# Performance work log

Hardware: AMD Instinct MI355X
Metric: run time of the kernel (lower is better)

Reference implementation:

```python
import jax, jax.numpy as jnp
import numpy as np

LOOKBACK = 1
LOOKAHEAD = 0
SEQ, BATCH, IN, HID = 1024, 16, 1024, 1024
K = LOOKBACK + 1 + LOOKAHEAD


def quick_gelu(x):
    return x * jax.nn.sigmoid(1.702 * x)


def setup_inputs() -> dict:
    key = jax.random.key(0)
    ks = jax.random.split(key, 5)
    scale = 1.0 / np.sqrt(IN * K)  # like torch Conv1d default init scale
    X = jax.random.normal(ks[0], (SEQ, BATCH, IN), dtype=jnp.float32)
    Wz = jax.random.normal(ks[1], (HID, IN, K), dtype=jnp.float32) * scale
    bz = jax.random.normal(ks[2], (HID,), dtype=jnp.float32) * scale
    Wf = jax.random.normal(ks[3], (HID, IN, K), dtype=jnp.float32) * scale
    bf = jax.random.normal(ks[4], (HID,), dtype=jnp.float32) * scale
    return {"X": X, "Wz": Wz, "bz": bz, "Wf": Wf, "bf": bf}


def _conv1d(x_pad, W, b):
    # x_pad: (B, Cin, T+K-1), W: (Cout, Cin, K) -> (B, Cout, T)
    y = jax.lax.conv_general_dilated(
        x_pad, W, window_strides=(1,), padding="VALID",
        dimension_numbers=("NCH", "OIH", "NCH"))
    return y + b[None, :, None]


def reference(X, Wz, bz, Wf, bf):
    # pad time dim: lookback zeros before, lookahead zeros after
    X_pad = jnp.pad(X, ((LOOKBACK, LOOKAHEAD), (0, 0), (0, 0)))
    X_pad = jnp.transpose(X_pad, (1, 2, 0))  # (B, Cin, T+K-1)
    Z = jnp.transpose(_conv1d(X_pad, Wz, bz), (2, 0, 1))  # (T, B, H)
    F = jnp.transpose(_conv1d(X_pad, Wf, bf), (2, 0, 1))  # (T, B, H)
    Z = quick_gelu(Z)
    F = jax.nn.sigmoid(F)

    def step(h, fz):
        f, z = fz
        h = f * z + (1.0 - f) * h
        return h, h

    h0 = jnp.zeros((BATCH, HID), dtype=X.dtype)
    _, H = jax.lax.scan(step, h0, (F, Z))  # H: (T, B, HID)
    return H, H[-1:, :, :]
```

## Files before the change

kernel.cpp:

```cpp
#include <hip/hip_runtime.h>
#include <stdint.h>

#define T_SEQ 1024
#define B_SZ  16
#define C_IN  1024
#define C_HID 1024
#define M_ROWS (T_SEQ * B_SZ)
#define N_COLS (2 * C_HID)
#define K_DIM  (2 * C_IN)

#define NCHUNK 16
#define CLEN   (T_SEQ / NCHUNK)
#define NBH    (B_SZ * C_HID)

typedef __attribute__((ext_vector_type(8))) short bf16x8;
typedef __attribute__((ext_vector_type(4))) float f32x4;
typedef unsigned short u16;

#define MFMA __builtin_amdgcn_mfma_f32_16x16x32_bf16

__device__ __forceinline__ u16 f2bf(float f) {
  union { float f; unsigned u; } v; v.f = f;
  unsigned r = v.u + 0x7fffu + ((v.u >> 16) & 1u);
  return (u16)(r >> 16);
}
__device__ __forceinline__ float bf2f(unsigned s) {
  union { unsigned u; float f; } v; v.u = s << 16;
  return v.f;
}

__device__ __forceinline__ void async_cp16(const u16* g, u16* l) {
  __builtin_amdgcn_global_load_lds(
      (const __attribute__((address_space(1))) unsigned*)(uintptr_t)g,
      (__attribute__((address_space(3))) unsigned*)(uintptr_t)l,
      16, 0, 0);
}

__global__ void k_convert_x(const float* __restrict__ X, u16* __restrict__ Xp) {
  int i = blockIdx.x * 256 + threadIdx.x;
  const int total4 = (M_ROWS + B_SZ) * C_IN / 4;
  if (i >= total4) return;
  int e = i << 2;
  const int PAD = B_SZ * C_IN;
  ushort4 o;
  if (e < PAD) {
    o.x = o.y = o.z = o.w = 0;
  } else {
    float4 v = *reinterpret_cast<const float4*>(X + (e - PAD));
    o.x = f2bf(v.x); o.y = f2bf(v.y); o.z = f2bf(v.z); o.w = f2bf(v.w);
  }
  *reinterpret_cast<ushort4*>(Xp + e) = o;
}

__global__ void k_repack_w(const float* __restrict__ Wz, const float* __restrict__ Wf,
                           u16* __restrict__ Wt) {
  int i = blockIdx.x * 256 + threadIdx.x;
  if (i >= 2 * 1024 * 1024) return;
  int g  = i >> 20;
  int hc = i & ((1 << 20) - 1);
  int h  = hc >> 10;
  int c  = hc & 1023;
  const float* W = g ? Wf : Wz;
  float2 w = *reinterpret_cast<const float2*>(W + ((size_t)(h << 10) + c) * 2);
  size_t n = ((size_t)h << 1) | (size_t)g;
  Wt[n * K_DIM + c]        = f2bf(w.x);
  Wt[n * K_DIM + 1024 + c] = f2bf(w.y);
}

__global__ __launch_bounds__(512, 2) void k_gemm8(const u16* __restrict__ Xp,
                                                  const u16* __restrict__ Wt,
                                                  const float* __restrict__ bz,
                                                  const float* __restrict__ bfv,
                                                  u16* __restrict__ Cb) {
  __shared__ u16 lds[2][2][2][8192];
  const int tid  = threadIdx.x;
  const int lane = tid & 63;
  const int wid  = tid >> 6;
  const int wr = wid >> 2;
  const int wc = wid & 3;
  const int lr = lane & 15;

  int wg = (blockIdx.x & 7) * 64 + (blockIdx.x >> 3);
  const int m0 = (wg >> 3) << 8;
  const int n0 = (wg & 7) << 8;

  const int p    = tid << 4;
  const int q    = p ^ (((p >> 7) & 7) << 4);
  const int grow = q >> 7;
  const int gcol = (q & 127) >> 1;
  const int ldsw = (tid >> 6) << 9;

  const int rbase = lr << 6;
  int co[2];
#pragma unroll
  for (int ks = 0; ks < 2; ++ks)
    co[ks] = ((((ks << 6) | ((lane >> 4) << 4)) ^ ((lr & 7) << 4)) >> 1);

  auto stage = [&](int j) {
    int kt = j >> 2, part = j & 3, buf = kt & 1;
    if (part >= 2) {
      int h = part - 2;
      const u16* g = Xp + (size_t)(m0 + (h << 7) + grow + ((kt >= 16) ? B_SZ : 0)) * C_IN
                        + ((kt & 15) << 6) + gcol;
      u16* l = &lds[buf][0][h][ldsw];
      async_cp16(g, l);
      async_cp16(g + (size_t)64 * C_IN, l + 4096);
    } else {
      const u16* g = Wt + (size_t)(n0 + (part << 7) + grow) * K_DIM + (kt << 6) + gcol;
      u16* l = &lds[buf][1][part][ldsw];
      async_cp16(g, l);
      async_cp16(g + (size_t)64 * K_DIM, l + 4096);
    }
  };

  f32x4 acc[8][4] = {};
  bf16x8 a[4][2], b0[2][2], b1[2][2];

  for (int j = 0; j < 7; ++j) stage(j);
  asm volatile("s_waitcnt vmcnt(6)" ::: "memory");
  __builtin_amdgcn_s_barrier();

#pragma unroll 2
  for (int t = 0; t < 32; ++t) {
    const int buf = t & 1;
    const u16* pA = &lds[buf][0][wr][0];
    const u16* pB = &lds[buf][1][wc >> 1][(wc & 1) << 12];
    const int jb = 4 * t + 7;

#pragma unroll
    for (int mi = 0; mi < 4; ++mi)
#pragma unroll
      for (int ks = 0; ks < 2; ++ks)
        a[mi][ks] = *(const bf16x8*)(pA + (mi << 10) + rbase + co[ks]);
#pragma unroll
    for (int ni = 0; ni < 2; ++ni)
#pragma unroll
      for (int ks = 0; ks < 2; ++ks)
        b0[ni][ks] = *(const bf16x8*)(pB + (ni << 10) + rbase + co[ks]);
    if (jb < 128) stage(jb);
    __builtin_amdgcn_s_barrier();
    asm volatile("s_waitcnt lgkmcnt(0)" ::: "memory");
    __builtin_amdgcn_s_setprio(1);
#pragma unroll
    for (int mi = 0; mi < 4; ++mi)
#pragma unroll
      for (int ni = 0; ni < 2; ++ni)
#pragma unroll
        for (int ks = 0; ks < 2; ++ks)
          acc[mi][ni] = MFMA(a[mi][ks], b0[ni][ks], acc[mi][ni], 0, 0, 0);
    __builtin_amdgcn_s_setprio(0);
    __builtin_amdgcn_s_barrier();

#pragma unroll
    for (int ni = 0; ni < 2; ++ni)
#pragma unroll
      for (int ks = 0; ks < 2; ++ks)
        b1[ni][ks] = *(const bf16x8*)(pB + ((2 + ni) << 10) + rbase + co[ks]);
    if (jb + 1 < 128) stage(jb + 1);
    __builtin_amdgcn_s_barrier();
    asm volatile("s_waitcnt lgkmcnt(0)" ::: "memory");
    __builtin_amdgcn_s_setprio(1);
#pragma unroll
    for (int mi = 0; mi < 4; ++mi)
#pragma unroll
      for (int ni = 0; ni < 2; ++ni)
#pragma unroll
        for (int ks = 0; ks < 2; ++ks)
          acc[mi][2 + ni] = MFMA(a[mi][ks], b1[ni][ks], acc[mi][2 + ni], 0, 0, 0);
    __builtin_amdgcn_s_setprio(0);
    __builtin_amdgcn_s_barrier();

#pragma unroll
    for (int mi = 0; mi < 4; ++mi)
#pragma unroll
      for (int ks = 0; ks < 2; ++ks)
        a[mi][ks] = *(const bf16x8*)(pA + ((4 + mi) << 10) + rbase + co[ks]);
    if (jb + 2 < 128) stage(jb + 2);
    __builtin_amdgcn_s_barrier();
    asm volatile("s_waitcnt lgkmcnt(0)" ::: "memory");
    __builtin_amdgcn_s_setprio(1);
#pragma unroll
    for (int mi = 0; mi < 4; ++mi)
#pragma unroll
      for (int ni = 0; ni < 2; ++ni)
#pragma unroll
        for (int ks = 0; ks < 2; ++ks)
          acc[4 + mi][2 + ni] = MFMA(a[mi][ks], b1[ni][ks], acc[4 + mi][2 + ni], 0, 0, 0);
    __builtin_amdgcn_s_setprio(0);
    __builtin_amdgcn_s_barrier();

    if (jb + 3 < 128) stage(jb + 3);
    if (t < 30) asm volatile("s_waitcnt vmcnt(6)" ::: "memory");
    else        asm volatile("s_waitcnt vmcnt(0)" ::: "memory");
    __builtin_amdgcn_s_barrier();
    __builtin_amdgcn_s_setprio(1);
#pragma unroll
    for (int mi = 0; mi < 4; ++mi)
#pragma unroll
      for (int ni = 0; ni < 2; ++ni)
#pragma unroll
        for (int ks = 0; ks < 2; ++ks)
          acc[4 + mi][ni] = MFMA(a[mi][ks], b0[ni][ks], acc[4 + mi][ni], 0, 0, 0);
    __builtin_amdgcn_s_setprio(0);
    __builtin_amdgcn_s_barrier();
  }

  const int colp = lane & 15;
  const bool isz = (colp & 1) == 0;
  const float kk = isz ? 1.702f : 1.0f;
  const int hbase = (n0 + (wc << 6) + colp) >> 1;
  const int fmb = (m0 >> 4) + (wr << 3);
  const int fnb = (n0 >> 4) + (wc << 2);
#pragma unroll
  for (int ni = 0; ni < 4; ++ni) {
    float bias = isz ? bz[hbase + 8 * ni] : bfv[hbase + 8 * ni];
#pragma unroll
    for (int mi = 0; mi < 8; ++mi) {
      ushort4 o;
#pragma unroll
      for (int r = 0; r < 4; ++r) {
        float v = acc[mi][ni][r] + bias;
        float s = 1.f / (1.f + __expf(-kk * v));
        ((u16*)&o)[r] = f2bf(isz ? v * s : s);
      }
      size_t fi = (size_t)(fmb + mi) * 128 + (fnb + ni);
      *reinterpret_cast<ushort4*>(Cb + fi * 256 + (lane << 2)) = o;
    }
  }
}

__global__ __launch_bounds__(256) void k_scan1(const u16* __restrict__ Cb,
                                               float* __restrict__ Ap,
                                               float* __restrict__ Bp) {
  int i = blockIdx.x * 256 + threadIdx.x;
  int h  = i & (C_HID - 1);
  int b4 = (i >> 10) & 3;
  int c  = i >> 12;
  const size_t lane_off = (size_t)(h >> 3) * 256 + b4 * 64 + (h & 7) * 8;
  float hh[4] = {0.f, 0.f, 0.f, 0.f}, P[4] = {1.f, 1.f, 1.f, 1.f};
#pragma unroll 8
  for (int tt = 0; tt < CLEN; ++tt) {
    size_t t = (size_t)c * CLEN + tt;
    uint4 v = *reinterpret_cast<const uint4*>(Cb + t * 32768 + lane_off);
    float z[4] = {bf2f(v.x & 0xffffu), bf2f(v.x >> 16),
                  bf2f(v.y & 0xffffu), bf2f(v.y >> 16)};
    float f[4] = {bf2f(v.z & 0xffffu), bf2f(v.z >> 16),
                  bf2f(v.w & 0xffffu), bf2f(v.w >> 16)};
#pragma unroll
    for (int r = 0; r < 4; ++r) {
      hh[r] += f[r] * (z[r] - hh[r]);
      P[r]  *= (1.f - f[r]);
    }
  }
  *reinterpret_cast<f32x4*>(Ap + (size_t)i * 4) = (f32x4){hh[0], hh[1], hh[2], hh[3]};
  *reinterpret_cast<f32x4*>(Bp + (size_t)i * 4) = (f32x4){P[0], P[1], P[2], P[3]};
}

__global__ __launch_bounds__(256) void k_scan2(const float* __restrict__ Ap,
                                               const float* __restrict__ Bp,
                                               float* __restrict__ St) {
  int j = blockIdx.x * 256 + threadIdx.x;
  float hh[4] = {0.f, 0.f, 0.f, 0.f};
#pragma unroll
  for (int c = 0; c < NCHUNK; ++c) {
    size_t idx = ((size_t)c * 4096 + j) * 4;
    *reinterpret_cast<f32x4*>(St + idx) = (f32x4){hh[0], hh[1], hh[2], hh[3]};
    f32x4 A = *reinterpret_cast<const f32x4*>(Ap + idx);
    f32x4 B = *reinterpret_cast<const f32x4*>(Bp + idx);
#pragma unroll
    for (int r = 0; r < 4; ++r) hh[r] = A[r] + B[r] * hh[r];
  }
}

__global__ __launch_bounds__(256) void k_scan3(const u16* __restrict__ Cb,
                                               const float* __restrict__ St,
                                               float* __restrict__ out) {
  int i = blockIdx.x * 256 + threadIdx.x;
  int h  = i & (C_HID - 1);
  int b4 = (i >> 10) & 3;
  int c  = i >> 12;
  const size_t lane_off = (size_t)(h >> 3) * 256 + b4 * 64 + (h & 7) * 8;
  f32x4 s = *reinterpret_cast<const f32x4*>(St + (size_t)i * 4);
  float hh[4] = {s[0], s[1], s[2], s[3]};
#pragma unroll 8
  for (int tt = 0; tt < CLEN; ++tt) {
    size_t t = (size_t)c * CLEN + tt;
    uint4 v = *reinterpret_cast<const uint4*>(Cb + t * 32768 + lane_off);
    float z[4] = {bf2f(v.x & 0xffffu), bf2f(v.x >> 16),
                  bf2f(v.y & 0xffffu), bf2f(v.y >> 16)};
    float f[4] = {bf2f(v.z & 0xffffu), bf2f(v.z >> 16),
                  bf2f(v.w & 0xffffu), bf2f(v.w >> 16)};
    float* op = out + t * 16384 + (size_t)b4 * 4096 + h;
#pragma unroll
    for (int r = 0; r < 4; ++r) {
      hh[r] += f[r] * (z[r] - hh[r]);
      op[r * 1024] = hh[r];
    }
  }
  if (c == NCHUNK - 1) {
    float* tp = out + (size_t)M_ROWS * C_HID + (size_t)b4 * 4096 + h;
#pragma unroll
    for (int r = 0; r < 4; ++r) tp[r * 1024] = hh[r];
  }
}

extern "C" void kernel_launch(void* const* d_in, const int* in_sizes, int n_in,
                              void* d_out, int out_size, void* d_ws, size_t ws_size,
                              hipStream_t stream) {
  const float* X   = (const float*)d_in[0];
  const float* Wz  = (const float*)d_in[1];
  const float* bz  = (const float*)d_in[2];
  const float* Wf  = (const float*)d_in[3];
  const float* bf_ = (const float*)d_in[4];
  float* out = (float*)d_out;

  u16* Xp = (u16*)d_ws;
  u16* Wt = Xp + (size_t)(M_ROWS + B_SZ) * C_IN;
  u16* Cb = Wt + (size_t)N_COLS * K_DIM;
  float* Ap = (float*)Xp;
  float* Bp = Ap + (size_t)NCHUNK * NBH;
  float* St = Bp + (size_t)NCHUNK * NBH;

  hipLaunchKernelGGL(k_convert_x, dim3(16400), dim3(256), 0, stream, X, Xp);
  hipLaunchKernelGGL(k_repack_w, dim3(8192), dim3(256), 0, stream, Wz, Wf, Wt);
  hipLaunchKernelGGL(k_gemm8, dim3((M_ROWS / 256) * (N_COLS / 256)), dim3(512), 0,
                     stream, Xp, Wt, bz, bf_, Cb);
  hipLaunchKernelGGL(k_scan1, dim3(256), dim3(256), 0, stream, Cb, Ap, Bp);
  hipLaunchKernelGGL(k_scan2, dim3(16), dim3(256), 0, stream, Ap, Bp, St);
  hipLaunchKernelGGL(k_scan3, dim3(256), dim3(256), 0, stream, Cb, St, out);
}
```

Measured before the change: 296.9 us.

## Single-buffer GEMM LDS for higher occupancy, merge prep kernels, fold scan2 into scan3

The GEMM drops the double-buffered LDS pipeline in favour of a single buffer, halving shared memory so launch bounds can request 4 blocks per SM. Each k-tile is now loaded with a full vmcnt(0) wait and barrier, and relies on other resident blocks to hide latency. The convert and repack kernels are merged into one launch, and the chunk-carry scan2 kernel is removed: each scan3 thread recomputes its prefix from the chunk summaries, which adds redundant serial work to later chunks. The single buffer means loads for the next tile are issued while the last MFMA group still reads registers; the barrier before staging has to protect LDS reuse, and the loss of prefetch overlap within a block could hurt.

```diff
diff --git a/kernel.cpp b/kernel.cpp
--- a/kernel.cpp
+++ b/kernel.cpp
@@ -36,43 +36,47 @@
       16, 0, 0);
 }
 
-__global__ void k_convert_x(const float* __restrict__ X, u16* __restrict__ Xp) {
-  int i = blockIdx.x * 256 + threadIdx.x;
-  const int total4 = (M_ROWS + B_SZ) * C_IN / 4;
-  if (i >= total4) return;
-  int e = i << 2;
-  const int PAD = B_SZ * C_IN;
-  ushort4 o;
-  if (e < PAD) {
-    o.x = o.y = o.z = o.w = 0;
+__global__ __launch_bounds__(256) void k_prep(const float* __restrict__ X,
+                                              const float* __restrict__ Wz,
+                                              const float* __restrict__ Wf,
+                                              u16* __restrict__ Xp,
+                                              u16* __restrict__ Wt) {
+  int blk = blockIdx.x;
+  if (blk < 16400) {
+    int i = blk * 256 + threadIdx.x;
+    const int total4 = (M_ROWS + B_SZ) * C_IN / 4;
+    if (i >= total4) return;
+    int e = i << 2;
+    const int PAD = B_SZ * C_IN;
+    ushort4 o;
+    if (e < PAD) {
+      o.x = o.y = o.z = o.w = 0;
+    } else {
+      float4 v = *reinterpret_cast<const float4*>(X + (e - PAD));
+      o.x = f2bf(v.x); o.y = f2bf(v.y); o.z = f2bf(v.z); o.w = f2bf(v.w);
+    }
+    *reinterpret_cast<ushort4*>(Xp + e) = o;
   } else {
-    float4 v = *reinterpret_cast<const float4*>(X + (e - PAD));
-    o.x = f2bf(v.x); o.y = f2bf(v.y); o.z = f2bf(v.z); o.w = f2bf(v.w);
-  }
-  *reinterpret_cast<ushort4*>(Xp + e) = o;
-}
-
-__global__ void k_repack_w(const float* __restrict__ Wz, const float* __restrict__ Wf,
-                           u16* __restrict__ Wt) {
-  int i = blockIdx.x * 256 + threadIdx.x;
-  if (i >= 2 * 1024 * 1024) return;
-  int g  = i >> 20;
-  int hc = i & ((1 << 20) - 1);
-  int h  = hc >> 10;
-  int c  = hc & 1023;
-  const float* W = g ? Wf : Wz;
-  float2 w = *reinterpret_cast<const float2*>(W + ((size_t)(h << 10) + c) * 2);
-  size_t n = ((size_t)h << 1) | (size_t)g;
-  Wt[n * K_DIM + c]        = f2bf(w.x);
-  Wt[n * K_DIM + 1024 + c] = f2bf(w.y);
-}
-
-__global__ __launch_bounds__(512, 2) void k_gemm8(const u16* __restrict__ Xp,
+    int i = (blk - 16400) * 256 + threadIdx.x;
+    if (i >= 2 * 1024 * 1024) return;
+    int g  = i >> 20;
+    int hc = i & ((1 << 20) - 1);
+    int h  = hc >> 10;
+    int c  = hc & 1023;
+    const float* W = g ? Wf : Wz;
+    float2 w = *reinterpret_cast<const float2*>(W + ((size_t)(h << 10) + c) * 2);
+    size_t n = ((size_t)h << 1) | (size_t)g;
+    Wt[n * K_DIM + c]        = f2bf(w.x);
+    Wt[n * K_DIM + 1024 + c] = f2bf(w.y);
+  }
+}
+
+__global__ __launch_bounds__(512, 4) void k_gemm8(const u16* __restrict__ Xp,
                                                   const u16* __restrict__ Wt,
                                                   const float* __restrict__ bz,
                                                   const float* __restrict__ bfv,
                                                   u16* __restrict__ Cb) {
-  __shared__ u16 lds[2][2][2][8192];
+  __shared__ u16 lds[2][2][8192];
   const int tid  = threadIdx.x;
   const int lane = tid & 63;
   const int wid  = tid >> 6;
@@ -96,18 +100,19 @@
   for (int ks = 0; ks < 2; ++ks)
     co[ks] = ((((ks << 6) | ((lane >> 4) << 4)) ^ ((lr & 7) << 4)) >> 1);
 
-  auto stage = [&](int j) {
-    int kt = j >> 2, part = j & 3, buf = kt & 1;
-    if (part >= 2) {
-      int h = part - 2;
+  auto stage = [&](int kt) {
+#pragma unroll
+    for (int h = 0; h < 2; ++h) {
       const u16* g = Xp + (size_t)(m0 + (h << 7) + grow + ((kt >= 16) ? B_SZ : 0)) * C_IN
                         + ((kt & 15) << 6) + gcol;
-      u16* l = &lds[buf][0][h][ldsw];
+      u16* l = &lds[0][h][ldsw];
       async_cp16(g, l);
       async_cp16(g + (size_t)64 * C_IN, l + 4096);
-    } else {
-      const u16* g = Wt + (size_t)(n0 + (part << 7) + grow) * K_DIM + (kt << 6) + gcol;
-      u16* l = &lds[buf][1][part][ldsw];
+    }
+#pragma unroll
+    for (int pp = 0; pp < 2; ++pp) {
+      const u16* g = Wt + (size_t)(n0 + (pp << 7) + grow) * K_DIM + (kt << 6) + gcol;
+      u16* l = &lds[1][pp][ldsw];
       async_cp16(g, l);
       async_cp16(g + (size_t)64 * K_DIM, l + 4096);
     }
@@ -116,16 +121,14 @@
   f32x4 acc[8][4] = {};
   bf16x8 a[4][2], b0[2][2], b1[2][2];
 
-  for (int j = 0; j < 7; ++j) stage(j);
-  asm volatile("s_waitcnt vmcnt(6)" ::: "memory");
-  __builtin_amdgcn_s_barrier();
-
-#pragma unroll 2
+  stage(0);
+
+  const u16* pA = &lds[0][wr][0];
+  const u16* pB = &lds[1][wc >> 1][(wc & 1) << 12];
+
   for (int t = 0; t < 32; ++t) {
-    const int buf = t & 1;
-    const u16* pA = &lds[buf][0][wr][0];
-    const u16* pB = &lds[buf][1][wc >> 1][(wc & 1) << 12];
-    const int jb = 4 * t + 7;
+    asm volatile("s_waitcnt vmcnt(0)" ::: "memory");
+    __builtin_amdgcn_s_barrier();
 
 #pragma unroll
     for (int mi = 0; mi < 4; ++mi)
@@ -137,8 +140,6 @@
 #pragma unroll
       for (int ks = 0; ks < 2; ++ks)
         b0[ni][ks] = *(const bf16x8*)(pB + (ni << 10) + rbase + co[ks]);
-    if (jb < 128) stage(jb);
-    __builtin_amdgcn_s_barrier();
     asm volatile("s_waitcnt lgkmcnt(0)" ::: "memory");
     __builtin_amdgcn_s_setprio(1);
 #pragma unroll
@@ -149,15 +150,12 @@
         for (int ks = 0; ks < 2; ++ks)
           acc[mi][ni] = MFMA(a[mi][ks], b0[ni][ks], acc[mi][ni], 0, 0, 0);
     __builtin_amdgcn_s_setprio(0);
-    __builtin_amdgcn_s_barrier();
 
 #pragma unroll
     for (int ni = 0; ni < 2; ++ni)
 #pragma unroll
       for (int ks = 0; ks < 2; ++ks)
         b1[ni][ks] = *(const bf16x8*)(pB + ((2 + ni) << 10) + rbase + co[ks]);
-    if (jb + 1 < 128) stage(jb + 1);
-    __builtin_amdgcn_s_barrier();
     asm volatile("s_waitcnt lgkmcnt(0)" ::: "memory");
     __builtin_amdgcn_s_setprio(1);
 #pragma unroll
@@ -168,15 +166,12 @@
         for (int ks = 0; ks < 2; ++ks)
           acc[mi][2 + ni] = MFMA(a[mi][ks], b1[ni][ks], acc[mi][2 + ni], 0, 0, 0);
     __builtin_amdgcn_s_setprio(0);
-    __builtin_amdgcn_s_barrier();
 
 #pragma unroll
     for (int mi = 0; mi < 4; ++mi)
 #pragma unroll
       for (int ks = 0; ks < 2; ++ks)
         a[mi][ks] = *(const bf16x8*)(pA + ((4 + mi) << 10) + rbase + co[ks]);
-    if (jb + 2 < 128) stage(jb + 2);
-    __builtin_amdgcn_s_barrier();
     asm volatile("s_waitcnt lgkmcnt(0)" ::: "memory");
     __builtin_amdgcn_s_setprio(1);
 #pragma unroll
@@ -187,12 +182,10 @@
         for (int ks = 0; ks < 2; ++ks)
           acc[4 + mi][2 + ni] = MFMA(a[mi][ks], b1[ni][ks], acc[4 + mi][2 + ni], 0, 0, 0);
     __builtin_amdgcn_s_setprio(0);
+
     __builtin_amdgcn_s_barrier();
-
-    if (jb + 3 < 128) stage(jb + 3);
-    if (t < 30) asm volatile("s_waitcnt vmcnt(6)" ::: "memory");
-    else        asm volatile("s_waitcnt vmcnt(0)" ::: "memory");
-    __builtin_amdgcn_s_barrier();
+    if (t < 31) stage(t + 1);
+
     __builtin_amdgcn_s_setprio(1);
 #pragma unroll
     for (int mi = 0; mi < 4; ++mi)
@@ -202,7 +195,6 @@
         for (int ks = 0; ks < 2; ++ks)
           acc[4 + mi][ni] = MFMA(a[mi][ks], b0[ni][ks], acc[4 + mi][ni], 0, 0, 0);
     __builtin_amdgcn_s_setprio(0);
-    __builtin_amdgcn_s_barrier();
   }
 
   const int colp = lane & 15;
@@ -256,32 +248,24 @@
   *reinterpret_cast<f32x4*>(Bp + (size_t)i * 4) = (f32x4){P[0], P[1], P[2], P[3]};
 }
 
-__global__ __launch_bounds__(256) void k_scan2(const float* __restrict__ Ap,
+__global__ __launch_bounds__(256) void k_scan3(const u16* __restrict__ Cb,
+                                               const float* __restrict__ Ap,
                                                const float* __restrict__ Bp,
-                                               float* __restrict__ St) {
-  int j = blockIdx.x * 256 + threadIdx.x;
-  float hh[4] = {0.f, 0.f, 0.f, 0.f};
-#pragma unroll
-  for (int c = 0; c < NCHUNK; ++c) {
-    size_t idx = ((size_t)c * 4096 + j) * 4;
-    *reinterpret_cast<f32x4*>(St + idx) = (f32x4){hh[0], hh[1], hh[2], hh[3]};
-    f32x4 A = *reinterpret_cast<const f32x4*>(Ap + idx);
-    f32x4 B = *reinterpret_cast<const f32x4*>(Bp + idx);
-#pragma unroll
-    for (int r = 0; r < 4; ++r) hh[r] = A[r] + B[r] * hh[r];
-  }
-}
-
-__global__ __launch_bounds__(256) void k_scan3(const u16* __restrict__ Cb,
-                                               const float* __restrict__ St,
                                                float* __restrict__ out) {
   int i = blockIdx.x * 256 + threadIdx.x;
   int h  = i & (C_HID - 1);
   int b4 = (i >> 10) & 3;
   int c  = i >> 12;
+  int j  = i & 4095;
+  float hh[4] = {0.f, 0.f, 0.f, 0.f};
+  for (int cc = 0; cc < c; ++cc) {
+    size_t idx = ((size_t)cc * 4096 + j) * 4;
+    f32x4 A = *reinterpret_cast<const f32x4*>(Ap + idx);
+    f32x4 B = *reinterpret_cast<const f32x4*>(Bp + idx);
+#pragma unroll
+    for (int r = 0; r < 4; ++r) hh[r] = A[r] + B[r] * hh[r];
+  }
   const size_t lane_off = (size_t)(h >> 3) * 256 + b4 * 64 + (h & 7) * 8;
-  f32x4 s = *reinterpret_cast<const f32x4*>(St + (size_t)i * 4);
-  float hh[4] = {s[0], s[1], s[2], s[3]};
 #pragma unroll 8
   for (int tt = 0; tt < CLEN; ++tt) {
     size_t t = (size_t)c * CLEN + tt;
@@ -319,13 +303,11 @@
   u16* Cb = Wt + (size_t)N_COLS * K_DIM;
   float* Ap = (float*)Xp;
   float* Bp = Ap + (size_t)NCHUNK * NBH;
-  float* St = Bp + (size_t)NCHUNK * NBH;
-
-  hipLaunchKernelGGL(k_convert_x, dim3(16400), dim3(256), 0, stream, X, Xp);
-  hipLaunchKernelGGL(k_repack_w, dim3(8192), dim3(256), 0, stream, Wz, Wf, Wt);
+
+  hipLaunchKernelGGL(k_prep, dim3(16400 + 8192), dim3(256), 0, stream,
+                     X, Wz, Wf, Xp, Wt);
   hipLaunchKernelGGL(k_gemm8, dim3((M_ROWS / 256) * (N_COLS / 256)), dim3(512), 0,
                      stream, Xp, Wt, bz, bf_, Cb);
   hipLaunchKernelGGL(k_scan1, dim3(256), dim3(256), 0, stream, Cb, Ap, Bp);
-  hipLaunchKernelGGL(k_scan2, dim3(16), dim3(256), 0, stream, Ap, Bp, St);
-  hipLaunchKernelGGL(k_scan3, dim3(256), dim3(256), 0, stream, Cb, St, out);
-}
+  hipLaunchKernelGGL(k_scan3, dim3(256), dim3(256), 0, stream, Cb, Ap, Bp, out);
+}
```

Measured after the change: 978.6 us. +229.6%, slower.

## Merge prep kernels, quadruple scan chunks, fold chunk-carry scan into final pass

Applied to the files above, without the earlier changes.

Combines the X conversion and weight repack into one launch. Raises the number of time chunks in the chunked linear-recurrence scan from 16 to 64, so the two scan passes launch 1024 blocks instead of 256. Removes the separate carry-propagation kernel: each thread in the final pass recomputes its incoming state by serially combining the earlier chunks' (A, B) pairs. This cuts two launches and exposes more parallelism on the bandwidth-bound scans, at the cost of redundant carry work that grows with chunk index.

```diff
diff --git a/kernel.cpp b/kernel.cpp
--- a/kernel.cpp
+++ b/kernel.cpp
@@ -9,7 +9,7 @@
 #define N_COLS (2 * C_HID)
 #define K_DIM  (2 * C_IN)
 
-#define NCHUNK 16
+#define NCHUNK 64
 #define CLEN   (T_SEQ / NCHUNK)
 #define NBH    (B_SZ * C_HID)
 
@@ -36,35 +36,39 @@
       16, 0, 0);
 }
 
-__global__ void k_convert_x(const float* __restrict__ X, u16* __restrict__ Xp) {
-  int i = blockIdx.x * 256 + threadIdx.x;
-  const int total4 = (M_ROWS + B_SZ) * C_IN / 4;
-  if (i >= total4) return;
-  int e = i << 2;
-  const int PAD = B_SZ * C_IN;
-  ushort4 o;
-  if (e < PAD) {
-    o.x = o.y = o.z = o.w = 0;
+__global__ __launch_bounds__(256) void k_prep(const float* __restrict__ X,
+                                              const float* __restrict__ Wz,
+                                              const float* __restrict__ Wf,
+                                              u16* __restrict__ Xp,
+                                              u16* __restrict__ Wt) {
+  int blk = blockIdx.x;
+  if (blk < 16400) {
+    int i = blk * 256 + threadIdx.x;
+    const int total4 = (M_ROWS + B_SZ) * C_IN / 4;
+    if (i >= total4) return;
+    int e = i << 2;
+    const int PAD = B_SZ * C_IN;
+    ushort4 o;
+    if (e < PAD) {
+      o.x = o.y = o.z = o.w = 0;
+    } else {
+      float4 v = *reinterpret_cast<const float4*>(X + (e - PAD));
+      o.x = f2bf(v.x); o.y = f2bf(v.y); o.z = f2bf(v.z); o.w = f2bf(v.w);
+    }
+    *reinterpret_cast<ushort4*>(Xp + e) = o;
   } else {
-    float4 v = *reinterpret_cast<const float4*>(X + (e - PAD));
-    o.x = f2bf(v.x); o.y = f2bf(v.y); o.z = f2bf(v.z); o.w = f2bf(v.w);
-  }
-  *reinterpret_cast<ushort4*>(Xp + e) = o;
-}
-
-__global__ void k_repack_w(const float* __restrict__ Wz, const float* __restrict__ Wf,
-                           u16* __restrict__ Wt) {
-  int i = blockIdx.x * 256 + threadIdx.x;
-  if (i >= 2 * 1024 * 1024) return;
-  int g  = i >> 20;
-  int hc = i & ((1 << 20) - 1);
-  int h  = hc >> 10;
-  int c  = hc & 1023;
-  const float* W = g ? Wf : Wz;
-  float2 w = *reinterpret_cast<const float2*>(W + ((size_t)(h << 10) + c) * 2);
-  size_t n = ((size_t)h << 1) | (size_t)g;
-  Wt[n * K_DIM + c]        = f2bf(w.x);
-  Wt[n * K_DIM + 1024 + c] = f2bf(w.y);
+    int i = (blk - 16400) * 256 + threadIdx.x;
+    if (i >= 2 * 1024 * 1024) return;
+    int g  = i >> 20;
+    int hc = i & ((1 << 20) - 1);
+    int h  = hc >> 10;
+    int c  = hc & 1023;
+    const float* W = g ? Wf : Wz;
+    float2 w = *reinterpret_cast<const float2*>(W + ((size_t)(h << 10) + c) * 2);
+    size_t n = ((size_t)h << 1) | (size_t)g;
+    Wt[n * K_DIM + c]        = f2bf(w.x);
+    Wt[n * K_DIM + 1024 + c] = f2bf(w.y);
+  }
 }
 
 __global__ __launch_bounds__(512, 2) void k_gemm8(const u16* __restrict__ Xp,
@@ -256,32 +260,24 @@
   *reinterpret_cast<f32x4*>(Bp + (size_t)i * 4) = (f32x4){P[0], P[1], P[2], P[3]};
 }
 
-__global__ __launch_bounds__(256) void k_scan2(const float* __restrict__ Ap,
+__global__ __launch_bounds__(256) void k_scan3(const u16* __restrict__ Cb,
+                                               const float* __restrict__ Ap,
                                                const float* __restrict__ Bp,
-                                               float* __restrict__ St) {
-  int j = blockIdx.x * 256 + threadIdx.x;
-  float hh[4] = {0.f, 0.f, 0.f, 0.f};
-#pragma unroll
-  for (int c = 0; c < NCHUNK; ++c) {
-    size_t idx = ((size_t)c * 4096 + j) * 4;
-    *reinterpret_cast<f32x4*>(St + idx) = (f32x4){hh[0], hh[1], hh[2], hh[3]};
-    f32x4 A = *reinterpret_cast<const f32x4*>(Ap + idx);
-    f32x4 B = *reinterpret_cast<const f32x4*>(Bp + idx);
-#pragma unroll
-    for (int r = 0; r < 4; ++r) hh[r] = A[r] + B[r] * hh[r];
-  }
-}
-
-__global__ __launch_bounds__(256) void k_scan3(const u16* __restrict__ Cb,
-                                               const float* __restrict__ St,
                                                float* __restrict__ out) {
   int i = blockIdx.x * 256 + threadIdx.x;
   int h  = i & (C_HID - 1);
   int b4 = (i >> 10) & 3;
   int c  = i >> 12;
+  int j  = i & 4095;
+  float hh[4] = {0.f, 0.f, 0.f, 0.f};
+  for (int cc = 0; cc < c; ++cc) {
+    size_t idx = ((size_t)cc * 4096 + j) * 4;
+    f32x4 A = *reinterpret_cast<const f32x4*>(Ap + idx);
+    f32x4 B = *reinterpret_cast<const f32x4*>(Bp + idx);
+#pragma unroll
+    for (int r = 0; r < 4; ++r) hh[r] = A[r] + B[r] * hh[r];
+  }
   const size_t lane_off = (size_t)(h >> 3) * 256 + b4 * 64 + (h & 7) * 8;
-  f32x4 s = *reinterpret_cast<const f32x4*>(St + (size_t)i * 4);
-  float hh[4] = {s[0], s[1], s[2], s[3]};
 #pragma unroll 8
   for (int tt = 0; tt < CLEN; ++tt) {
     size_t t = (size_t)c * CLEN + tt;
@@ -319,13 +315,13 @@
   u16* Cb = Wt + (size_t)N_COLS * K_DIM;
   float* Ap = (float*)Xp;
   float* Bp = Ap + (size_t)NCHUNK * NBH;
-  float* St = Bp + (size_t)NCHUNK * NBH;
-
-  hipLaunchKernelGGL(k_convert_x, dim3(16400), dim3(256), 0, stream, X, Xp);
-  hipLaunchKernelGGL(k_repack_w, dim3(8192), dim3(256), 0, stream, Wz, Wf, Wt);
+
+  hipLaunchKernelGGL(k_prep, dim3(16400 + 8192), dim3(256), 0, stream,
+                     X, Wz, Wf, Xp, Wt);
   hipLaunchKernelGGL(k_gemm8, dim3((M_ROWS / 256) * (N_COLS / 256)), dim3(512), 0,
                      stream, Xp, Wt, bz, bf_, Cb);
-  hipLaunchKernelGGL(k_scan1, dim3(256), dim3(256), 0, stream, Cb, Ap, Bp);
-  hipLaunchKernelGGL(k_scan2, dim3(16), dim3(256), 0, stream, Ap, Bp, St);
-  hipLaunchKernelGGL(k_scan3, dim3(256), dim3(256), 0, stream, Cb, St, out);
-}
+  hipLaunchKernelGGL(k_scan1, dim3(NCHUNK * 4096 / 256), dim3(256), 0, stream,
+                     Cb, Ap, Bp);
+  hipLaunchKernelGGL(k_scan3, dim3(NCHUNK * 4096 / 256), dim3(256), 0, stream,
+                     Cb, Ap, Bp, out);
+}
```

New measurement: 299.9 us. About the same (+1.0%).
